# Kernel optimization log

Measured on AMD Instinct MI355X. Metric: run time of the kernel, lower is better.

## Reference

```python
import jax, jax.numpy as jnp
import numpy as np

B, L, E, H = 4, 2048, 1024, 16
D = E // H  # head_dim = 64
NEG_INF = -1e9


def _rope(x):
    # x: [B, L, H, D]; standard rotate-half RoPE over head_dim
    seq = x.shape[1]
    inv_freq = 1.0 / (10000.0 ** (jnp.arange(0, D, 2, dtype=jnp.float32) / D))  # [D/2]
    ang = jnp.arange(seq, dtype=jnp.float32)[:, None] * inv_freq               # [L, D/2]
    cos = jnp.concatenate([jnp.cos(ang), jnp.cos(ang)], axis=-1)[None, :, None, :]
    sin = jnp.concatenate([jnp.sin(ang), jnp.sin(ang)], axis=-1)[None, :, None, :]
    x1, x2 = jnp.split(x, 2, axis=-1)
    rot = jnp.concatenate([-x2, x1], axis=-1)
    return x * cos + rot * sin


def setup_inputs() -> dict:
    key = jax.random.key(0)
    ks = jax.random.split(key, 12)
    xavier = lambda k: jax.random.uniform(k, (E, E), jnp.float32,
                                          -np.sqrt(6.0 / (E + E)), np.sqrt(6.0 / (E + E)))
    return {
        "query": jax.random.normal(ks[0], (B, L, E), jnp.float32),
        "key": jax.random.normal(ks[1], (B, L, E), jnp.float32),
        "value": jax.random.normal(ks[2], (B, L, E), jnp.float32),
        "wq": xavier(ks[3]), "bq": jnp.zeros((E,), jnp.float32),
        "wk": xavier(ks[4]), "bk": jnp.zeros((E,), jnp.float32),
        "wv": xavier(ks[5]), "bv": jnp.zeros((E,), jnp.float32),
        "wo": xavier(ks[6]), "bo": jnp.zeros((E,), jnp.float32),
        "key_padding_mask": jax.random.randint(ks[7], (B, L), 0, 2).astype(bool),
    }


def reference(query, key, value, wq, bq, wk, bk, wv, bv, wo, bo, key_padding_mask):
    b, ql = query.shape[0], query.shape[1]
    sl = key.shape[1]
    q = (query @ wq.T + bq).reshape(b, ql, H, D)
    k = (key @ wk.T + bk).reshape(b, sl, H, D)
    v = (value @ wv.T + bv).reshape(b, sl, H, D)
    q = _rope(q)
    k = _rope(k)
    # causal mask (is_causal=True, attn_mask=None path) + key padding mask, additive
    causal = jnp.where(jnp.triu(jnp.ones((ql, sl), bool), k=1), NEG_INF, 0.0)  # [L, L]
    kpm = jnp.where(key_padding_mask[:, None, None, :], NEG_INF, 0.0)          # [B,1,1,S]
    mask = causal[None, None, :, :] + kpm
    scores = jnp.einsum("bqhd,bkhd->bhqk", q, k) / np.sqrt(D) + mask
    attn = jax.nn.softmax(scores, axis=-1)
    out = jnp.einsum("bhqk,bkhd->bqhd", attn, v).reshape(b, ql, E)
    return out @ wo.T + bo
```

## Files before the change

kernel.cpp:

```cpp
#include <hip/hip_runtime.h>

typedef unsigned short u16;
typedef unsigned int   u32;

using bf16x8 = __attribute__((ext_vector_type(8))) __bf16;
using f32x4  = __attribute__((ext_vector_type(4))) float;
using f32x16 = __attribute__((ext_vector_type(16))) float;
using u32x4  = __attribute__((ext_vector_type(4))) u32;

#define DEV static __device__ __forceinline__
#define GP(p) (const __attribute__((address_space(1))) void*)(p)
#define LP(p) (__attribute__((address_space(3))) void*)(p)
#define WAITB(N) asm volatile("s_waitcnt vmcnt(" N ")\n\ts_barrier" ::: "memory")
#define WAITVM(N) do{ asm volatile("s_waitcnt vmcnt(" N ")" ::: "memory"); \
                      __builtin_amdgcn_sched_barrier(0); }while(0)
#define LGKMB asm volatile("s_waitcnt lgkmcnt(0)\n\ts_barrier" ::: "memory")

DEV u16 f2bf(float f){
  u32 u = __builtin_bit_cast(u32, f);
  u32 r = u + 0x7fffu + ((u>>16)&1u);
  return (u16)(r>>16);
}
DEV float bcf(u32 x){ return __builtin_bit_cast(float, x); }
DEV bf16x8 as_bf(uint4 v){ return __builtin_bit_cast(bf16x8, v); }
DEV u32 cvt_pk(float lo, float hi){
  u32 r;
  asm("v_cvt_pk_bf16_f32 %0, %1, %2" : "=v"(r) : "v"(lo), "v"(hi));
  return r;
}
DEV void plswap(u32 &a, u32 &b){
  auto r = __builtin_amdgcn_permlane32_swap((int)a, (int)b, false, false);
  a = (u32)r[0]; b = (u32)r[1];
}
DEV float fexp2(float x){ float r; asm("v_exp_f32 %0, %1" : "=v"(r) : "v"(x)); return r; }
DEV float max3f(float a, float b, float c){
  float r; asm("v_max3_f32 %0, %1, %2, %3" : "=v"(r) : "v"(a), "v"(b), "v"(c)); return r;
}
DEV float fractf_(float x){ float r; asm("v_fract_f32 %0, %1" : "=v"(r) : "v"(x)); return r; }
DEV float sinrev(float f){ float r; asm("v_sin_f32 %0, %1" : "=v"(r) : "v"(f)); return r; }
DEV float cosrev(float f){ float r; asm("v_cos_f32 %0, %1" : "=v"(r) : "v"(f)); return r; }

constexpr int CB = 4, CL = 2048, CE = 1024, CH = 16, CD = 64;
constexpr int CM = CB*CL;
constexpr float LOG2E  = 1.44269504088896f;
constexpr float NEGBIG = -1.44269504e9f;
constexpr float INV2PI = 0.15915494309189535f;

__global__ void detect_mask_kernel(const void* __restrict__ mask, int* __restrict__ flag){
  __shared__ int a_gt1, a_badf, a_oddnz, a_evennz;
  if (threadIdx.x==0){ a_gt1=0; a_badf=0; a_oddnz=0; a_evennz=0; }
  __syncthreads();
  const u32* w = (const u32*)mask;
  int gt1=0, badf=0, oddnz=0, evennz=0;
  for (int i=threadIdx.x; i<2048; i+=256){
    u32 v = w[i];
    if (v > 1u) gt1 = 1;
    if (v != 0u && v != 0x3f800000u) badf = 1;
    if (v != 0u){ if (i & 1) oddnz = 1; else evennz = 1; }
  }
  if (gt1) atomicOr(&a_gt1,1);
  if (badf) atomicOr(&a_badf,1);
  if (oddnz) atomicOr(&a_oddnz,1);
  if (evennz) atomicOr(&a_evennz,1);
  __syncthreads();
  if (threadIdx.x==0){
    int mode;
    if (!a_gt1)           mode = (!a_oddnz && a_evennz) ? 3 : 0;
    else if (!a_badf)     mode = 1;
    else                  mode = 2;
    flag[0] = mode;
  }
}

__global__ void convert_mask_kernel(const void* __restrict__ mask, const int* __restrict__ flag,
                                    float* __restrict__ maskf){
  int i = blockIdx.x*blockDim.x + threadIdx.x;
  if (i >= CB*CL) return;
  int mode = flag[0];
  int v;
  if      (mode==0) v = ((const int*)mask)[i] != 0;
  else if (mode==1) v = ((const float*)mask)[i] != 0.f;
  else if (mode==3) v = ((const int*)mask)[2*i] != 0;
  else              v = ((const unsigned char*)mask)[i] != 0;
  maskf[i] = v ? NEGBIG : 0.f;
}

__global__ __launch_bounds__(512) void gemm_qkv(
    const float* __restrict__ query, const float* __restrict__ keyp,
    const float* __restrict__ value,
    const float* __restrict__ wq, const float* __restrict__ wk,
    const float* __restrict__ wv,
    const float* __restrict__ bq, const float* __restrict__ bk, const float* __restrict__ bv,
    u16* __restrict__ Qp, u16* __restrict__ Kp, u16* __restrict__ Vt)
{
  __shared__ u16 As[2][16384];
  __shared__ u16 Bs[2][8192];
  const int z = blockIdx.y;
  const int tid=threadIdx.x, lane=tid&63, wid=tid>>6;
  const int llo=lane&15, lhi=lane>>4;
  const float* Af; const float* Btf;
  if (z==0){ Af=query; Btf=wq; }
  else if (z==1){ Af=keyp; Btf=wk; }
  else { Af=wv; Btf=value; }
  int bid = blockIdx.x;
  int xcd = bid&7, j = bid>>3;
  int mb, nb;
  if (z<2){ mb = xcd*4 + (j>>3); nb = j&7; }
  else    { mb = j&3;  nb = xcd*8 + (j>>2); }
  const int m0 = mb*256, n0 = nb*128;
  const int wr = wid>>1, wc = wid&1;
  const int rswA = llo&7;

  const float* aptr[4]; int aco[4];
  #pragma unroll
  for (int i=0;i<4;i++){
    int c = tid + i*512, row=c>>3, sc=(c&7)^(row&7);
    aptr[i] = Af + (size_t)(m0+row)*CE + sc*8;
    aco[i] = c*8;
  }
  const float* bptr[2]; int bco[2];
  #pragma unroll
  for (int i=0;i<2;i++){
    int c = tid + i*512, row=c>>3, sc=(c&7)^(row&7);
    bptr[i] = Btf + (size_t)(n0+row)*CE + sc*8;
    bco[i] = c*8;
  }

  u32x4 A0[8], B0[4], A1[8], B1[4];

#define LOADT(T, RA, RB) do{ \
  _Pragma("unroll") \
  for (int i=0;i<4;i++){ \
    asm volatile("global_load_dwordx4 %0, %2, off\n\tglobal_load_dwordx4 %1, %2, off offset:16" \
      : "=&v"(RA[2*i]), "=&v"(RA[2*i+1]) : "v"(aptr[i] + (size_t)(T)*64) : "memory"); \
  } \
  _Pragma("unroll") \
  for (int i=0;i<2;i++){ \
    asm volatile("global_load_dwordx4 %0, %2, off\n\tglobal_load_dwordx4 %1, %2, off offset:16" \
      : "=&v"(RB[2*i]), "=&v"(RB[2*i+1]) : "v"(bptr[i] + (size_t)(T)*64) : "memory"); \
  } \
}while(0)

#define CVTW(dst, lo4, hi4) do{ \
  dst.x = cvt_pk(bcf(lo4.x), bcf(lo4.y)); \
  dst.y = cvt_pk(bcf(lo4.z), bcf(lo4.w)); \
  dst.z = cvt_pk(bcf(hi4.x), bcf(hi4.y)); \
  dst.w = cvt_pk(bcf(hi4.z), bcf(hi4.w)); \
}while(0)

#define WRITET(BUF, RA, RB) do{ \
  _Pragma("unroll") \
  for (int i=0;i<4;i++){ \
    u32x4 w; CVTW(w, RA[2*i], RA[2*i+1]); \
    *(u32x4*)&As[BUF][aco[i]] = w; \
  } \
  _Pragma("unroll") \
  for (int i=0;i<2;i++){ \
    u32x4 w; CVTW(w, RB[2*i], RB[2*i+1]); \
    *(u32x4*)&Bs[BUF][bco[i]] = w; \
  } \
}while(0)

  f32x4 acc[4][4] = {};

  auto COMP = [&](int buf){
    const char* as = (const char*)As[buf];
    const char* bs = (const char*)Bs[buf];
    #pragma unroll
    for (int ks=0; ks<2; ks++){
      bf16x8 af[4], bf_[4];
      #pragma unroll
      for (int mr=0;mr<4;mr++){
        int r = wr*64+mr*16+llo;
        af[mr] = as_bf(*(const uint4*)(as + r*128 + (((ks*4+lhi)^rswA)<<4)));
      }
      #pragma unroll
      for (int nr=0;nr<4;nr++){
        int r = wc*64+nr*16+llo;
        bf_[nr] = as_bf(*(const uint4*)(bs + r*128 + (((ks*4+lhi)^rswA)<<4)));
      }
      #pragma unroll
      for (int mr=0;mr<4;mr++)
        #pragma unroll
        for (int nr=0;nr<4;nr++)
          acc[mr][nr] = __builtin_amdgcn_mfma_f32_16x16x32_bf16(af[mr], bf_[nr], acc[mr][nr], 0,0,0);
    }
  };

  LOADT(0, A0, B0);
  LOADT(1, A1, B1);
  WAITVM("12");
  WRITET(0, A0, B0);
  LGKMB;

  #pragma unroll 1
  for (int jj=0; jj<7; jj++){
    const int t = 2*jj;
    LOADT(t+2, A0, B0);
    COMP(0);
    WAITVM("12");
    WRITET(1, A1, B1);
    LGKMB;
    LOADT(t+3, A1, B1);
    COMP(1);
    WAITVM("12");
    WRITET(0, A0, B0);
    LGKMB;
  }
  COMP(0);
  WAITVM("0");
  WRITET(1, A1, B1);
  LGKMB;
  COMP(1);

#undef LOADT
#undef WRITET

  const int colbase = n0 + wc*64;
  if (z < 2){
    const float* bias = z ? bk : bq;
    u16* outp = z ? Kp : Qp;
    const float scale = z ? 1.f : 0.125f*LOG2E;
    const int h = colbase >> 6;
    float b1[2], b2[2], invr[2];
    #pragma unroll
    for (int nr=0;nr<2;nr++){
      int j2 = nr*16 + llo;
      b1[nr] = bias[colbase + j2];
      b2[nr] = bias[colbase + j2 + 32];
      invr[nr] = exp2f(-(float)j2 * 0.41524101186092033f) * INV2PI;
    }
    #pragma unroll
    for (int mr=0;mr<4;mr++)
      #pragma unroll
      for (int r=0;r<4;r++){
        int row = m0 + wr*64 + mr*16 + lhi*4 + r;
        int b = row >> 11, l = row & 2047;
        u16* dst = outp + (((size_t)(b*CH + h)*CL + l) << 6);
        #pragma unroll
        for (int nr=0;nr<2;nr++){
          int j2 = nr*16 + llo;
          float x1 = (acc[mr][nr][r]   + b1[nr]) * scale;
          float x2 = (acc[mr][nr+2][r] + b2[nr]) * scale;
          float fr = fractf_((float)l * invr[nr]);
          float sn = sinrev(fr), cs = cosrev(fr);
          dst[j2]      = f2bf(x1*cs - x2*sn);
          dst[j2 + 32] = f2bf(x2*cs + x1*sn);
        }
      }
  } else {
    #pragma unroll
    for (int mr=0;mr<4;mr++)
      #pragma unroll
      for (int r=0;r<4;r++){
        int row = m0 + wr*64 + mr*16 + lhi*4 + r;
        float bvv = bv[row];
        #pragma unroll
        for (int nr=0;nr<4;nr++){
          int col = colbase + nr*16 + llo;
          Vt[(size_t)row*CM + col] = f2bf(acc[mr][nr][r] + bvv);
        }
      }
  }
}

__global__ __launch_bounds__(512) void gemm_out(
    const u16* __restrict__ A, const float* __restrict__ Btf,
    const float* __restrict__ bias, float* __restrict__ C)
{
  __shared__ u16 As[3][16384];
  __shared__ u16 Bs[2][8192];
  const int tid=threadIdx.x, lane=tid&63, wid=tid>>6;
  const int llo=lane&15, lhi=lane>>4;
  int bid = blockIdx.x;
  int xcd = bid&7, j = bid>>3;
  const int m0 = (xcd*4 + (j>>3))*256, n0 = (j&7)*128;
  const int wr = wid>>1, wc = wid&1;
  const int rswA = llo&7;

  auto STAGEA = [&](int t, int buf){
    #pragma unroll
    for (int i=0;i<4;i++){
      int c = tid + i*512, row=c>>3, sc=(c&7)^(row&7);
      __builtin_amdgcn_global_load_lds(GP(A + (size_t)(m0+row)*CE + t*64 + sc*8),
                                       LP(&As[buf][c*8]), 16, 0, 0);
    }
  };

  const float* bptr[2]; int bco[2];
  #pragma unroll
  for (int i=0;i<2;i++){
    int c = tid + i*512, row=c>>3, sc=(c&7)^(row&7);
    bptr[i] = Btf + (size_t)(n0+row)*CE + sc*8;
    bco[i] = c*8;
  }
  u32x4 B0[4], B1[4];

#define LOADB(T, RB) do{ \
  _Pragma("unroll") \
  for (int i=0;i<2;i++){ \
    asm volatile("global_load_dwordx4 %0, %2, off\n\tglobal_load_dwordx4 %1, %2, off offset:16" \
      : "=&v"(RB[2*i]), "=&v"(RB[2*i+1]) : "v"(bptr[i] + (size_t)(T)*64) : "memory"); \
  } \
}while(0)

#define WRITEB(BUF, RB) do{ \
  _Pragma("unroll") \
  for (int i=0;i<2;i++){ \
    u32x4 w; CVTW(w, RB[2*i], RB[2*i+1]); \
    *(u32x4*)&Bs[BUF][bco[i]] = w; \
  } \
}while(0)

  f32x4 acc[4][4] = {};

  auto COMP = [&](int abuf, int bbuf){
    const char* as = (const char*)As[abuf];
    const char* bs = (const char*)Bs[bbuf];
    #pragma unroll
    for (int ks=0; ks<2; ks++){
      bf16x8 af[4], bf_[4];
      #pragma unroll
      for (int mr=0;mr<4;mr++){
        int r = wr*64+mr*16+llo;
        af[mr] = as_bf(*(const uint4*)(as + r*128 + (((ks*4+lhi)^rswA)<<4)));
      }
      #pragma unroll
      for (int nr=0;nr<4;nr++){
        int r = wc*64+nr*16+llo;
        bf_[nr] = as_bf(*(const uint4*)(bs + r*128 + (((ks*4+lhi)^rswA)<<4)));
      }
      #pragma unroll
      for (int mr=0;mr<4;mr++)
        #pragma unroll
        for (int nr=0;nr<4;nr++)
          acc[mr][nr] = __builtin_amdgcn_mfma_f32_16x16x32_bf16(af[mr], bf_[nr], acc[mr][nr], 0,0,0);
    }
  };

  STAGEA(0,0); LOADB(0, B0);
  STAGEA(1,1); LOADB(1, B1);
  WAITVM("8");
  WRITEB(0, B0);
  LGKMB;

  #pragma unroll 1
  for (int jj=0; jj<7; jj++){
    const int t = 2*jj;
    STAGEA(t+2, (t+2)%3); LOADB(t+2, B0);
    COMP(t%3, 0);
    WAITVM("8");
    WRITEB(1, B1);
    LGKMB;
    STAGEA(t+3, (t+3)%3); LOADB(t+3, B1);
    COMP((t+1)%3, 1);
    WAITVM("8");
    WRITEB(0, B0);
    LGKMB;
  }
  COMP(2, 0);
  WAITVM("0");
  WRITEB(1, B1);
  LGKMB;
  COMP(0, 1);

#undef LOADB
#undef WRITEB

  #pragma unroll
  for (int mr=0;mr<4;mr++)
    #pragma unroll
    for (int nr=0;nr<4;nr++)
      #pragma unroll
      for (int r=0;r<4;r++){
        int row = m0 + wr*64 + mr*16 + lhi*4 + r;
        int col = n0 + wc*64 + nr*16 + llo;
        C[(size_t)row*CE + col] = acc[mr][nr][r] + bias[col];
      }
}

__global__ __launch_bounds__(256,2) void attn_kernel(
    const u16* __restrict__ Qp, const u16* __restrict__ Kp, const u16* __restrict__ Vt,
    const float* __restrict__ maskf, u16* __restrict__ AO)
{
  __shared__ u16 K_lds[4][4096];
  __shared__ u16 V_lds[4][4096];
  __shared__ float M_lds[2048];
  const int bh = blockIdx.x;
  const int slot = blockIdx.y;
  const int b = bh >> 4, h = bh & 15;
  const int tid=threadIdx.x, lane=tid&63, wid=tid>>6;
  const int l31 = lane&31, hi = lane>>5;
  const u16* Qh = Qp + (size_t)bh*CL*CD;
  const u16* Kh = Kp + (size_t)bh*CL*CD;
  const u16* Vhd = Vt + (size_t)(h*CD)*CM + b*CL;

  #pragma unroll
  for (int i=0;i<2;i++)
    __builtin_amdgcn_global_load_lds(GP(maskf + b*CL + (i*256+tid)*4),
                                     LP(&M_lds[(i*256+tid)*4]), 16, 0, 0);

  auto STAGE = [&](int t, int buf){
    const u16* Ksrc = Kh + t*64*CD;
    const u16* Vsrc = Vhd + t*64;
    #pragma unroll
    for (int i=0;i<2;i++){
      int c = tid + i*256;
      int row = c>>3, sc = c&7;
      int c16 = sc ^ (row&7);
      __builtin_amdgcn_global_load_lds(GP(Ksrc + row*CD + c16*8),
                                       LP(&K_lds[buf][c*8]), 16, 0, 0);
      __builtin_amdgcn_global_load_lds(GP(Vsrc + (size_t)row*CM + c16*8),
                                       LP(&V_lds[buf][c*8]), 16, 0, 0);
    }
  };

  const int rowb = l31*128;
  const int rsw  = (l31&7)<<4;
  const int qts2[2] = {15-slot, slot};

  for (int qi=0; qi<2; qi++){
    const int qt = qts2[qi];
    const int qw0 = qt*128 + wid*32;
    const int qlane = qw0 + l31;

    bf16x8 qf[4];
    #pragma unroll
    for (int c=0;c<4;c++)
      qf[c] = as_bf(*(const uint4*)(Qh + (size_t)qlane*CD + c*16 + hi*8));

    f32x16 o0 = {}, o1 = {};
    float m_r = -3e38f, l_r = 0.f;

    const int nt = qt*2 + 2;
    STAGE(0,0); STAGE(1,1);

    for (int t=0; t<nt; t++){
      if (t+2 < nt){ STAGE(t+2,(t+2)&3); WAITB("8"); }
      else if (t+1 < nt){ WAITB("4"); }
      else { WAITB("0"); }

      const int kv0 = t*64;
      const char* kb = (const char*)K_lds[t&3];
      const char* vb = (const char*)V_lds[t&3];

      f32x4 cm[8];
      #pragma unroll
      for (int s2=0;s2<2;s2++)
        #pragma unroll
        for (int g=0; g<4; g++)
          cm[s2*4+g] = *(const f32x4*)&M_lds[kv0 + s2*32 + g*8 + hi*4];

      f32x16 s0 = {}, s1 = {};
      __builtin_amdgcn_s_setprio(1);
      #pragma unroll
      for (int c=0;c<4;c++){
        int cb = (c*32 + hi*16) ^ rsw;
        bf16x8 k0 = as_bf(*(const uint4*)(kb + rowb + cb));
        bf16x8 k1 = as_bf(*(const uint4*)(kb + 4096 + rowb + cb));
        s0 = __builtin_amdgcn_mfma_f32_32x32x16_bf16(k0, qf[c], s0, 0,0,0);
        s1 = __builtin_amdgcn_mfma_f32_32x32x16_bf16(k1, qf[c], s1, 0,0,0);
      }
      __builtin_amdgcn_s_setprio(0);

      if (kv0 + 63 > qw0){
        #pragma unroll
        for (int s2=0;s2<2;s2++){
          f32x16& sv = s2 ? s1 : s0;
          #pragma unroll
          for (int reg=0; reg<16; reg++){
            int k = kv0 + s2*32 + (reg&3) + (reg>>2)*8 + hi*4;
            float v = sv[reg] + cm[s2*4+(reg>>2)][reg&3];
            sv[reg] = (k > qlane) ? v + NEGBIG : v;
          }
        }
      } else {
        #pragma unroll
        for (int s2=0;s2<2;s2++){
          f32x16& sv = s2 ? s1 : s0;
          #pragma unroll
          for (int reg=0; reg<16; reg++)
            sv[reg] = sv[reg] + cm[s2*4+(reg>>2)][reg&3];
        }
      }

      f32x16 mx;
      #pragma unroll
      for (int r=0;r<16;r++) mx[r] = fmaxf(s0[r], s1[r]);
      float a0 = max3f(mx[0],mx[1],mx[2]);
      float a1 = max3f(mx[3],mx[4],mx[5]);
      float a2 = max3f(mx[6],mx[7],mx[8]);
      float a3 = max3f(mx[9],mx[10],mx[11]);
      float a4 = max3f(mx[12],mx[13],mx[14]);
      float vmax = fmaxf(max3f(a0,a1,a2), max3f(a3,a4,mx[15]));
      vmax = fmaxf(vmax, __shfl_xor(vmax, 32));

      if (__any(vmax > m_r + 12.0f)){
        float mnew = fmaxf(m_r, vmax);
        float sc = fexp2(m_r - mnew);
        l_r *= sc;
        o0 *= sc; o1 *= sc;
        m_r = mnew;
      }

      #pragma unroll
      for (int r=0;r<16;r++){
        s0[r] = fexp2(s0[r] - m_r);
        s1[r] = fexp2(s1[r] - m_r);
      }
      f32x16 sm = s0 + s1;
      #pragma unroll
      for (int w=8; w>=1; w>>=1)
        #pragma unroll
        for (int r=0;r<w;r++) sm[r] = sm[r] + sm[r+w];
      float rsum = sm[0];
      rsum += __shfl_xor(rsum, 32);
      l_r += rsum;

      u32 w_[16];
      #pragma unroll
      for (int s2=0;s2<2;s2++){
        f32x16& sv = s2 ? s1 : s0;
        #pragma unroll
        for (int c=0;c<2;c++){
          u32 a  = cvt_pk(sv[c*8+0], sv[c*8+1]);
          u32 bb = cvt_pk(sv[c*8+2], sv[c*8+3]);
          u32 cc = cvt_pk(sv[c*8+4], sv[c*8+5]);
          u32 dd = cvt_pk(sv[c*8+6], sv[c*8+7]);
          plswap(a, cc); plswap(bb, dd);
          int base = (s2*2+c)*4;
          w_[base+0]=a; w_[base+1]=bb; w_[base+2]=cc; w_[base+3]=dd;
        }
      }

      __builtin_amdgcn_s_setprio(1);
      #pragma unroll
      for (int kc=0; kc<4; kc++){
        bf16x8 pf = as_bf(make_uint4(w_[kc*4], w_[kc*4+1], w_[kc*4+2], w_[kc*4+3]));
        int cb = (kc*32 + hi*16) ^ rsw;
        bf16x8 v0 = as_bf(*(const uint4*)(vb + rowb + cb));
        bf16x8 v1 = as_bf(*(const uint4*)(vb + 4096 + rowb + cb));
        o0 = __builtin_amdgcn_mfma_f32_32x32x16_bf16(v0, pf, o0, 0,0,0);
        o1 = __builtin_amdgcn_mfma_f32_32x32x16_bf16(v1, pf, o1, 0,0,0);
      }
      __builtin_amdgcn_s_setprio(0);
    }

    float inv = 1.f / l_r;
    u16* dst = AO + (size_t)(b*CL + qlane)*CE + h*CD;
    #pragma unroll
    for (int mt=0; mt<2; mt++){
      f32x16& ov = mt ? o1 : o0;
      #pragma unroll
      for (int g=0; g<4; g++){
        u32 lo  = cvt_pk(ov[g*4+0]*inv, ov[g*4+1]*inv);
        u32 hi2 = cvt_pk(ov[g*4+2]*inv, ov[g*4+3]*inv);
        *(uint2*)(dst + mt*32 + g*8 + hi*4) = make_uint2(lo, hi2);
      }
    }
    __syncthreads();
  }
}

extern "C" void kernel_launch(void* const* d_in, const int* in_sizes, int n_in,
                              void* d_out, int out_size, void* d_ws, size_t ws_size,
                              hipStream_t stream) {
  const float* query = (const float*)d_in[0];
  const float* key_  = (const float*)d_in[1];
  const float* value = (const float*)d_in[2];
  const float* wq = (const float*)d_in[3];
  const float* bq = (const float*)d_in[4];
  const float* wk = (const float*)d_in[5];
  const float* bk = (const float*)d_in[6];
  const float* wv = (const float*)d_in[7];
  const float* bv = (const float*)d_in[8];
  const float* wo = (const float*)d_in[9];
  const float* bo = (const float*)d_in[10];
  const void*  kpm = d_in[11];

  char* ws = (char*)d_ws;
  constexpr size_t SZ_ME_BF = (size_t)CM*CE*2;
  constexpr size_t OFF_FLAG = 0;
  constexpr size_t OFF_MASKF= 256;
  constexpr size_t OFF_AO   = 65536;
  constexpr size_t OFF_KP   = OFF_AO + SZ_ME_BF;
  constexpr size_t OFF_VT   = OFF_KP + SZ_ME_BF;
  constexpr size_t OFF_QP   = OFF_VT + SZ_ME_BF;

  int*   flag  = (int*)(ws + OFF_FLAG);
  float* maskf = (float*)(ws + OFF_MASKF);
  u16*  AO  = (u16*)(ws + OFF_AO);
  u16*  Kp  = (u16*)(ws + OFF_KP);
  u16*  Vt  = (u16*)(ws + OFF_VT);
  u16*  Qp  = (u16*)(ws + OFF_QP);

  detect_mask_kernel<<<1,256,0,stream>>>(kpm, flag);
  convert_mask_kernel<<<(CB*CL+255)/256,256,0,stream>>>(kpm, flag, maskf);

  gemm_qkv<<<dim3(256,3),512,0,stream>>>(query, key_, value, wq, wk, wv,
                                         bq, bk, bv, Qp, Kp, Vt);

  attn_kernel<<<dim3(CB*CH, 8),256,0,stream>>>(Qp, Kp, Vt, maskf, AO);

  gemm_out<<<256,512,0,stream>>>(AO, wo, bo, (float*)d_out);
}
```

Before: 192.7 us.

## Software-pipeline attention QK with softmax/PV, reorder GEMM compute, fuse mask kernels

The attention loop is restructured so the QK^T MFMAs for tile t run alongside the softmax and PV of tile t-1, using two score register sets. Both GEMM main loops now issue the LDS writes of the next tile before the current tile's MFMAs, so the stores overlap with compute. The two mask preprocessing kernels are merged into one launch in which each block repeats the format detection. The attention change raises register pressure and the double-buffer wait logic is more intricate.

```diff
diff --git a/kernel.cpp b/kernel.cpp
--- a/kernel.cpp
+++ b/kernel.cpp
@@ -46,7 +46,7 @@
 constexpr float NEGBIG = -1.44269504e9f;
 constexpr float INV2PI = 0.15915494309189535f;
 
-__global__ void detect_mask_kernel(const void* __restrict__ mask, int* __restrict__ flag){
+__global__ void mask_kernel(const void* __restrict__ mask, float* __restrict__ maskf){
   __shared__ int a_gt1, a_badf, a_oddnz, a_evennz;
   if (threadIdx.x==0){ a_gt1=0; a_badf=0; a_oddnz=0; a_evennz=0; }
   __syncthreads();
@@ -63,20 +63,11 @@
   if (oddnz) atomicOr(&a_oddnz,1);
   if (evennz) atomicOr(&a_evennz,1);
   __syncthreads();
-  if (threadIdx.x==0){
-    int mode;
-    if (!a_gt1)           mode = (!a_oddnz && a_evennz) ? 3 : 0;
-    else if (!a_badf)     mode = 1;
-    else                  mode = 2;
-    flag[0] = mode;
-  }
-}
-
-__global__ void convert_mask_kernel(const void* __restrict__ mask, const int* __restrict__ flag,
-                                    float* __restrict__ maskf){
+  int mode;
+  if (!a_gt1)           mode = (!a_oddnz && a_evennz) ? 3 : 0;
+  else if (!a_badf)     mode = 1;
+  else                  mode = 2;
   int i = blockIdx.x*blockDim.x + threadIdx.x;
-  if (i >= CB*CL) return;
-  int mode = flag[0];
   int v;
   if      (mode==0) v = ((const int*)mask)[i] != 0;
   else if (mode==1) v = ((const float*)mask)[i] != 0.f;
@@ -197,19 +188,19 @@
   for (int jj=0; jj<7; jj++){
     const int t = 2*jj;
     LOADT(t+2, A0, B0);
-    COMP(0);
     WAITVM("12");
     WRITET(1, A1, B1);
+    COMP(0);
     LGKMB;
     LOADT(t+3, A1, B1);
-    COMP(1);
     WAITVM("12");
     WRITET(0, A0, B0);
+    COMP(1);
     LGKMB;
   }
-  COMP(0);
   WAITVM("0");
   WRITET(1, A1, B1);
+  COMP(0);
   LGKMB;
   COMP(1);
 
@@ -348,19 +339,19 @@
   for (int jj=0; jj<7; jj++){
     const int t = 2*jj;
     STAGEA(t+2, (t+2)%3); LOADB(t+2, B0);
-    COMP(t%3, 0);
     WAITVM("8");
     WRITEB(1, B1);
+    COMP(t%3, 0);
     LGKMB;
     STAGEA(t+3, (t+3)%3); LOADB(t+3, B1);
-    COMP((t+1)%3, 1);
     WAITVM("8");
     WRITEB(0, B0);
+    COMP((t+1)%3, 1);
     LGKMB;
   }
-  COMP(2, 0);
   WAITVM("0");
   WRITEB(1, B1);
+  COMP(2, 0);
   LGKMB;
   COMP(0, 1);
 
@@ -431,37 +422,37 @@
 
     f32x16 o0 = {}, o1 = {};
     float m_r = -3e38f, l_r = 0.f;
+    f32x16 sA0, sA1, sB0, sB1;
 
     const int nt = qt*2 + 2;
     STAGE(0,0); STAGE(1,1);
 
-    for (int t=0; t<nt; t++){
-      if (t+2 < nt){ STAGE(t+2,(t+2)&3); WAITB("8"); }
-      else if (t+1 < nt){ WAITB("4"); }
-      else { WAITB("0"); }
-
-      const int kv0 = t*64;
+    auto QK = [&](int t, f32x16& d0, f32x16& d1){
       const char* kb = (const char*)K_lds[t&3];
-      const char* vb = (const char*)V_lds[t&3];
-
-      f32x4 cm[8];
-      #pragma unroll
-      for (int s2=0;s2<2;s2++)
-        #pragma unroll
-        for (int g=0; g<4; g++)
-          cm[s2*4+g] = *(const f32x4*)&M_lds[kv0 + s2*32 + g*8 + hi*4];
-
-      f32x16 s0 = {}, s1 = {};
+      f32x16 z0 = {}, z1 = {};
       __builtin_amdgcn_s_setprio(1);
       #pragma unroll
       for (int c=0;c<4;c++){
         int cb = (c*32 + hi*16) ^ rsw;
         bf16x8 k0 = as_bf(*(const uint4*)(kb + rowb + cb));
         bf16x8 k1 = as_bf(*(const uint4*)(kb + 4096 + rowb + cb));
-        s0 = __builtin_amdgcn_mfma_f32_32x32x16_bf16(k0, qf[c], s0, 0,0,0);
-        s1 = __builtin_amdgcn_mfma_f32_32x32x16_bf16(k1, qf[c], s1, 0,0,0);
+        z0 = __builtin_amdgcn_mfma_f32_32x32x16_bf16(k0, qf[c], z0, 0,0,0);
+        z1 = __builtin_amdgcn_mfma_f32_32x32x16_bf16(k1, qf[c], z1, 0,0,0);
       }
       __builtin_amdgcn_s_setprio(0);
+      d0 = z0; d1 = z1;
+    };
+
+    auto SMPV = [&](int tp, f32x16& s0, f32x16& s1){
+      const int kv0 = tp*64;
+      const char* vb = (const char*)V_lds[tp&3];
+
+      f32x4 cm[8];
+      #pragma unroll
+      for (int s2=0;s2<2;s2++)
+        #pragma unroll
+        for (int g=0; g<4; g++)
+          cm[s2*4+g] = *(const f32x4*)&M_lds[kv0 + s2*32 + g*8 + hi*4];
 
       if (kv0 + 63 > qw0){
         #pragma unroll
@@ -544,7 +535,29 @@
         o1 = __builtin_amdgcn_mfma_f32_32x32x16_bf16(v1, pf, o1, 0,0,0);
       }
       __builtin_amdgcn_s_setprio(0);
+    };
+
+    WAITB("4");
+    if (2 < nt) STAGE(2,2);
+    QK(0, sA0, sA1);
+
+    #pragma unroll 1
+    for (int jx=0; jx<qt; jx++){
+      int t = 2*jx+1;
+      WAITB("4");
+      if (t+2 < nt) STAGE(t+2,(t+2)&3);
+      QK(t, sB0, sB1);
+      SMPV(t-1, sA0, sA1);
+      t = 2*jx+2;
+      WAITB("4");
+      if (t+2 < nt) STAGE(t+2,(t+2)&3);
+      QK(t, sA0, sA1);
+      SMPV(t-1, sB0, sB1);
     }
+    WAITB("0");
+    QK(nt-1, sB0, sB1);
+    SMPV(nt-2, sA0, sA1);
+    SMPV(nt-1, sB0, sB1);
 
     float inv = 1.f / l_r;
     u16* dst = AO + (size_t)(b*CL + qlane)*CE + h*CD;
@@ -580,22 +593,19 @@
 
   char* ws = (char*)d_ws;
   constexpr size_t SZ_ME_BF = (size_t)CM*CE*2;
-  constexpr size_t OFF_FLAG = 0;
   constexpr size_t OFF_MASKF= 256;
   constexpr size_t OFF_AO   = 65536;
   constexpr size_t OFF_KP   = OFF_AO + SZ_ME_BF;
   constexpr size_t OFF_VT   = OFF_KP + SZ_ME_BF;
   constexpr size_t OFF_QP   = OFF_VT + SZ_ME_BF;
 
-  int*   flag  = (int*)(ws + OFF_FLAG);
   float* maskf = (float*)(ws + OFF_MASKF);
   u16*  AO  = (u16*)(ws + OFF_AO);
   u16*  Kp  = (u16*)(ws + OFF_KP);
   u16*  Vt  = (u16*)(ws + OFF_VT);
   u16*  Qp  = (u16*)(ws + OFF_QP);
 
-  detect_mask_kernel<<<1,256,0,stream>>>(kpm, flag);
-  convert_mask_kernel<<<(CB*CL+255)/256,256,0,stream>>>(kpm, flag, maskf);
+  mask_kernel<<<32,256,0,stream>>>(kpm, maskf);
 
   gemm_qkv<<<dim3(256,3),512,0,stream>>>(query, key_, value, wq, wk, wv,
                                          bq, bk, bv, Qp, Kp, Vt);
```

New measurement: 190.4 us. No clear change (-1.2%).
